# Performance work log

Hardware: AMD Instinct MI355X
Metric: run time of the kernel (lower is better)

Reference implementation:

```python
import jax, jax.numpy as jnp
import numpy as np

EPS = 1e-5  # torch BatchNorm2d default eps


def _conv(x, w, pad=0, groups=1):
    # x: NCHW, w: OIHW (torch layout); matches nn.Conv2d with given padding/groups
    return jax.lax.conv_general_dilated(
        x, w, window_strides=(1, 1), padding=[(pad, pad), (pad, pad)],
        dimension_numbers=("NCHW", "OIHW", "NCHW"), feature_group_count=groups)


def _bn_train(x, gamma, beta):
    # BatchNorm2d in training mode: batch stats over (N,H,W), biased variance
    m = jnp.mean(x, axis=(0, 2, 3), keepdims=True)
    v = jnp.mean(jnp.square(x - m), axis=(0, 2, 3), keepdims=True)
    return (x - m) * jax.lax.rsqrt(v + EPS) * gamma.reshape(1, -1, 1, 1) + beta.reshape(1, -1, 1, 1)


def setup_inputs() -> dict:
    key = jax.random.key(0)
    ks = jax.random.split(key, 8)
    B, C, H, W = 8, 32, 128, 128
    D = 8                      # num_directions
    WC = C * D                 # wavelet_channels = 256
    MID = WC * 2               # 512
    x = jax.random.normal(ks[0], (B, C, H, W), jnp.float32)
    # grouped directional filter bank: Conv2d(C, C*D, k=5, groups=C, bias=False)
    w_dir = jax.random.normal(ks[1], (WC, 1, 5, 5), jnp.float32) / np.sqrt(25.0)
    # wavelet_conv: Conv(WC->MID,3) BN ReLU Conv(MID->WC,3) BN ReLU
    w1 = jax.random.normal(ks[2], (MID, WC, 3, 3), jnp.float32) / np.sqrt(WC * 9.0)
    b1 = jnp.zeros((MID,), jnp.float32)
    g1 = jnp.ones((MID,), jnp.float32)
    be1 = jnp.zeros((MID,), jnp.float32)
    w2 = jax.random.normal(ks[3], (WC, MID, 3, 3), jnp.float32) / np.sqrt(MID * 9.0)
    b2 = jnp.zeros((WC,), jnp.float32)
    g2 = jnp.ones((WC,), jnp.float32)
    be2 = jnp.zeros((WC,), jnp.float32)
    # inverse_conv: Conv2d(WC, C, 1)
    w_inv = jax.random.normal(ks[4], (C, WC, 1, 1), jnp.float32) / np.sqrt(float(WC))
    b_inv = jnp.zeros((C,), jnp.float32)
    return {"x": x, "w_dir": w_dir, "w1": w1, "b1": b1, "g1": g1, "be1": be1,
            "w2": w2, "b2": b2, "g2": g2, "be2": be2, "w_inv": w_inv, "b_inv": b_inv}


def reference(x, w_dir, w1, b1, g1, be1, w2, b2, g2, be2, w_inv, b_inv):
    C = x.shape[1]
    # directional wavelet: grouped conv C -> C*8, k=5, pad=2, no bias
    coeffs = _conv(x, w_dir, pad=2, groups=C)                      # (B, 8C, H, W)
    # wavelet-domain conv stack
    h = _conv(coeffs, w1, pad=1) + b1.reshape(1, -1, 1, 1)         # (B, 16C, H, W)
    h = jax.nn.relu(_bn_train(h, g1, be1))
    h = _conv(h, w2, pad=1) + b2.reshape(1, -1, 1, 1)              # (B, 8C, H, W)
    h = jax.nn.relu(_bn_train(h, g2, be2))
    # inverse 1x1 conv back to C channels
    return _conv(h, w_inv) + b_inv.reshape(1, -1, 1, 1)            # (B, C, H, W)
```

## Files before the change

kernel.cpp:

```cpp
#include <hip/hip_runtime.h>

typedef unsigned short u16;
typedef unsigned int   u32;
typedef __attribute__((ext_vector_type(8)))  __bf16 bf16x8;
typedef __attribute__((ext_vector_type(4)))  float  f32x4;
typedef __attribute__((ext_vector_type(16))) float  f32x16;

__device__ __forceinline__ float bf2f(u16 u) {
    union { u32 i; float f; } v; v.i = ((u32)u) << 16; return v.f;
}
__device__ __forceinline__ u16 f2bf(float f) {
    u32 u = __float_as_uint(f);
    u32 r = (u + 0x7FFFu + ((u >> 16) & 1u)) >> 16;
    return (u16)r;
}

__device__ __forceinline__ void gl16(const u16* g, u16* l) {
    __builtin_amdgcn_global_load_lds(
        (const __attribute__((address_space(1))) unsigned int*)g,
        (__attribute__((address_space(3))) unsigned int*)l, 16, 0, 0);
}

__global__ __launch_bounds__(256) void dir_conv_k(const float* __restrict__ x,
                                                  const float* __restrict__ wd,
                                                  u16* __restrict__ coeffs) {
    int bid = blockIdx.x;
    int cc = bid & 3, y = (bid >> 2) & 127, n = bid >> 9;
    __shared__ float lx[5280];
    __shared__ float lw[1600];
    int t = threadIdx.x;
    for (int i = t; i < 1600; i += 256) {
        int ol = i / 25, tap = i - ol * 25;
        lw[tap * 64 + ol] = wd[(cc * 64 + ol) * 25 + tap];
    }
    for (int i = t; i < 5280; i += 256) {
        int c = i / 660, rem = i - c * 660;
        int ky = rem / 132, xx = rem - ky * 132;
        int gy = y - 2 + ky, gx = xx - 2;
        float v = 0.f;
        if (gy >= 0 && gy < 128 && gx >= 0 && gx < 128)
            v = x[(((n * 32 + cc * 8 + c) * 128 + gy) << 7) + gx];
        lx[i] = v;
    }
    __syncthreads();
    int px = t >> 1, oh = t & 1;
    float acc[4][8];
#pragma unroll
    for (int j = 0; j < 4; ++j)
#pragma unroll
        for (int d = 0; d < 8; ++d) acc[j][d] = 0.f;
#pragma unroll
    for (int j = 0; j < 4; ++j) {
        int cl = oh * 4 + j;
        const float* lxc = &lx[cl * 660];
#pragma unroll
        for (int ky = 0; ky < 5; ++ky)
#pragma unroll
            for (int kx = 0; kx < 5; ++kx) {
                float xv = lxc[ky * 132 + px + kx];
                const float* w8 = &lw[(ky * 5 + kx) * 64 + cl * 8];
#pragma unroll
                for (int d = 0; d < 8; ++d) acc[j][d] += xv * w8[d];
            }
    }
    long base = ((long)((n * 128 + y) * 128 + px)) * 256 + cc * 64 + oh * 32;
#pragma unroll
    for (int j = 0; j < 4; ++j) {
        uint4 o;
        o.x = (u32)f2bf(acc[j][0]) | ((u32)f2bf(acc[j][1]) << 16);
        o.y = (u32)f2bf(acc[j][2]) | ((u32)f2bf(acc[j][3]) << 16);
        o.z = (u32)f2bf(acc[j][4]) | ((u32)f2bf(acc[j][5]) << 16);
        o.w = (u32)f2bf(acc[j][6]) | ((u32)f2bf(acc[j][7]) << 16);
        *(uint4*)(coeffs + base + j * 8) = o;
    }
}

__global__ __launch_bounds__(256) void repack_w_k(const float* __restrict__ w,
                                                  u16* __restrict__ wp,
                                                  int OC, int IC, int total) {
    int f = blockIdx.x * 256 + threadIdx.x;
    if (f >= total) return;
    int KC = IC >> 5;
    int j  = f & 7;
    int h  = (f >> 3) & 1;
    int g  = f >> 4;
    int oc = g % OC; g /= OC;
    int s  = g & 1;  g >>= 1;
    int kc = g % KC;
    int tap = g / KC;
    int ic = kc * 32 + s * 16 + h * 8 + j;
    wp[f] = f2bf(w[(oc * IC + ic) * 9 + tap]);
}

template<int IC, int OC>
__global__ __launch_bounds__(256, 2) void conv3_k(const u16* __restrict__ base,
                                                  u32 in_off,
                                                  const u16* __restrict__ wp,
                                                  const float* __restrict__ bias,
                                                  u32 zp_off,
                                                  u16* __restrict__ outp,
                                                  float* __restrict__ statp) {
    constexpr int KC = IC / 32;
    constexpr int W  = 130;
    constexpr int TU = 12 * W;
    constexpr int NFULL = TU / 256;
    constexpr int REM   = TU % 256;
    __shared__ u16 lA0[TU * 8];
    __shared__ u16 lA1[TU * 8];

    int bx0 = blockIdx.x;
    int bx = ((bx0 & 7) << 7) + (bx0 >> 3);
    int y = bx & 127, n = bx >> 7;
    int ocb = blockIdx.y;
    int t = threadIdx.x, lane = t & 63, wv = t >> 6;
    int lm = lane & 31, h = lane >> 5;
    int ocw = ocb * 256 + wv * 64;

    u32 off[NFULL + 1];
#pragma unroll
    for (int i = 0; i <= NFULL; ++i) {
        int u = (i == NFULL) ? (NFULL * 256 + lane) : (i * 256 + t);
        int icq = u / (3 * W);
        int r2  = u - icq * (3 * W);
        int dy  = r2 / W;
        int xx  = r2 - dy * W;
        int gy = y - 1 + dy, gx = xx - 1;
        bool ok = ((unsigned)gy < 128u) && ((unsigned)gx < 128u);
        off[i] = ok ? (in_off + (u32)((n * 128 + gy) * 128 + gx) * IC + (icq & 3) * 8)
                    : zp_off;
    }

    auto stage = [&](u16* dst, int kc) {
#pragma unroll
        for (int i = 0; i < NFULL; ++i)
            gl16(base + off[i] + kc * 32, dst + (i * 256 + wv * 64) * 8);
        if (wv == 0 && lane < REM)
            gl16(base + off[NFULL] + kc * 32, dst + NFULL * 256 * 8);
    };

    u32 wboff = (u32)(ocw + lm) * 16 + h * 8;
    bf16x8 Ar[2][4];
    bf16x8 Br[2][2];

    {
        const u16* wb = wp + wboff;
        Br[0][0] = *(const bf16x8*)wb;
        Br[0][1] = *(const bf16x8*)(wb + 512);
    }

    f32x16 acc[4][2];
#pragma unroll
    for (int mf = 0; mf < 4; ++mf)
#pragma unroll
        for (int nf = 0; nf < 2; ++nf)
#pragma unroll
            for (int r = 0; r < 16; ++r) acc[mf][nf][r] = 0.f;

    stage(lA0, 0);
    for (int kc = 0; kc < KC; ++kc) {
        const u16* lAu = (kc & 1) ? lA1 : lA0;
        u16*       lAn = (kc & 1) ? lA0 : lA1;
        __syncthreads();
        {
            int au = ((h * 3) * W + lm) * 8;
            Ar[0][0] = *(const bf16x8*)(lAu + au);
            Ar[0][1] = *(const bf16x8*)(lAu + au + 256);
            Ar[0][2] = *(const bf16x8*)(lAu + au + 512);
            Ar[0][3] = *(const bf16x8*)(lAu + au + 768);
        }
        if (kc + 1 < KC) stage(lAn, kc + 1);
#pragma unroll
        for (int i = 0; i < 18; ++i) {
            const int j   = (i + 1) % 18;
            const int jdy = j / 6, jdx = (j % 6) >> 1, js = j & 1;
            const int jkc = (i == 17) ? ((kc + 1 < KC) ? kc + 1 : 0) : kc;
            if (i != 17) {
                int au = (((js * 2 + h) * 3 + jdy) * W + jdx + lm) * 8;
                Ar[j & 1][0] = *(const bf16x8*)(lAu + au);
                Ar[j & 1][1] = *(const bf16x8*)(lAu + au + 256);
                Ar[j & 1][2] = *(const bf16x8*)(lAu + au + 512);
                Ar[j & 1][3] = *(const bf16x8*)(lAu + au + 768);
            }
            {
                const u16* wb = wp + wboff
                    + (u32)(((jdy * 3 + jdx) * KC + jkc) * 2 + js) * (OC * 16);
                Br[j & 1][0] = *(const bf16x8*)wb;
                Br[j & 1][1] = *(const bf16x8*)(wb + 512);
            }
            __builtin_amdgcn_s_setprio(1);
            acc[0][0] = __builtin_amdgcn_mfma_f32_32x32x16_bf16(Ar[i & 1][0], Br[i & 1][0], acc[0][0], 0, 0, 0);
            acc[0][1] = __builtin_amdgcn_mfma_f32_32x32x16_bf16(Ar[i & 1][0], Br[i & 1][1], acc[0][1], 0, 0, 0);
            acc[1][0] = __builtin_amdgcn_mfma_f32_32x32x16_bf16(Ar[i & 1][1], Br[i & 1][0], acc[1][0], 0, 0, 0);
            acc[1][1] = __builtin_amdgcn_mfma_f32_32x32x16_bf16(Ar[i & 1][1], Br[i & 1][1], acc[1][1], 0, 0, 0);
            acc[2][0] = __builtin_amdgcn_mfma_f32_32x32x16_bf16(Ar[i & 1][2], Br[i & 1][0], acc[2][0], 0, 0, 0);
            acc[2][1] = __builtin_amdgcn_mfma_f32_32x32x16_bf16(Ar[i & 1][2], Br[i & 1][1], acc[2][1], 0, 0, 0);
            acc[3][0] = __builtin_amdgcn_mfma_f32_32x32x16_bf16(Ar[i & 1][3], Br[i & 1][0], acc[3][0], 0, 0, 0);
            acc[3][1] = __builtin_amdgcn_mfma_f32_32x32x16_bf16(Ar[i & 1][3], Br[i & 1][1], acc[3][1], 0, 0, 0);
            __builtin_amdgcn_s_setprio(0);
        }
    }

    long rowb = (long)(n * 128 + y) * 128;
    float ss[2] = {0.f, 0.f}, qq[2] = {0.f, 0.f};
#pragma unroll
    for (int nf = 0; nf < 2; ++nf) {
        int oc = ocw + nf * 32 + lm;
        float bi = bias[oc];
#pragma unroll
        for (int mf = 0; mf < 4; ++mf)
#pragma unroll
            for (int r = 0; r < 16; ++r) {
                int px = mf * 32 + (r & 3) + ((r >> 2) << 3) + (h << 2);
                u16 bv = f2bf(acc[mf][nf][r] + bi);
                outp[(rowb + px) * OC + oc] = bv;
                float vr = bf2f(bv);
                ss[nf] += vr;
                qq[nf] += vr * vr;
            }
    }
#pragma unroll
    for (int nf = 0; nf < 2; ++nf) {
        ss[nf] += __shfl_xor(ss[nf], 32);
        qq[nf] += __shfl_xor(qq[nf], 32);
    }
    if (h == 0) {
#pragma unroll
        for (int nf = 0; nf < 2; ++nf) {
            int oc = ocw + nf * 32 + lm;
            atomicAdd(&statp[oc * 2],     ss[nf]);
            atomicAdd(&statp[oc * 2 + 1], qq[nf]);
        }
    }
}

template<int C>
__global__ __launch_bounds__(256) void stats2_k(const float* __restrict__ part,
                                                const float* __restrict__ g,
                                                const float* __restrict__ be,
                                                float* __restrict__ ab) {
    int ch = blockIdx.x * 256 + threadIdx.x;
    if (ch >= C) return;
    float s = part[ch * 2], q = part[ch * 2 + 1];
    const float M = 131072.f;
    float mean = s / M;
    float var = q / M - mean * mean;
    float a = g[ch] * rsqrtf(var + 1e-5f);
    ab[ch * 2]     = a;
    ab[ch * 2 + 1] = be[ch] - mean * a;
}

__global__ __launch_bounds__(256) void bn_relu_k(u16* __restrict__ h,
                                                 const float* __restrict__ ab) {
    long idx8 = (long)blockIdx.x * 256 + threadIdx.x;
    u16* p = h + idx8 * 8;
    uint4 v = *(const uint4*)p;
    int chb = ((int)idx8 & 63) << 3;
    u32 w[4] = {v.x, v.y, v.z, v.w};
    u32 o[4];
#pragma unroll
    for (int q = 0; q < 4; ++q) {
        int ch = chb + q * 2;
        float2 a0 = *(const float2*)(ab + ch * 2);
        float2 a1 = *(const float2*)(ab + ch * 2 + 2);
        float f0 = bf2f((u16)(w[q] & 0xffff));
        float f1 = bf2f((u16)(w[q] >> 16));
        f0 = fmaxf(f0 * a0.x + a0.y, 0.f);
        f1 = fmaxf(f1 * a1.x + a1.y, 0.f);
        o[q] = (u32)f2bf(f0) | ((u32)f2bf(f1) << 16);
    }
    *(uint4*)p = make_uint4(o[0], o[1], o[2], o[3]);
}

__global__ __launch_bounds__(256) void inv_conv_k(const u16* __restrict__ h2,
                                                  const float* __restrict__ ab,
                                                  const float* __restrict__ winv,
                                                  const float* __restrict__ binv,
                                                  float* __restrict__ out) {
    __shared__ float lw[8192];
    __shared__ float lab[512];
    int t = threadIdx.x;
    for (int i = t; i < 8192; i += 256) {
        int k = i >> 5, oc = i & 31;
        lw[i] = winv[oc * 256 + k];
    }
    lab[t] = ab[t];
    lab[t + 256] = ab[t + 256];
    __syncthreads();
    long p = (long)blockIdx.x * 256 + t;
    const u16* hp = h2 + p * 256;
    f32x4 acc[8];
    f32x4 zero = {0.f, 0.f, 0.f, 0.f};
#pragma unroll
    for (int q = 0; q < 8; ++q) acc[q] = zero;
    for (int k = 0; k < 256; k += 8) {
        uint4 hv = *(const uint4*)(hp + k);
        u32 wv[4] = {hv.x, hv.y, hv.z, hv.w};
#pragma unroll
        for (int e = 0; e < 8; ++e) {
            u16 us = (e & 1) ? (u16)(wv[e >> 1] >> 16) : (u16)(wv[e >> 1] & 0xffff);
            int kk = k + e;
            float v = bf2f(us);
            v = fmaxf(v * lab[kk * 2] + lab[kk * 2 + 1], 0.f);
            const f32x4* w4 = (const f32x4*)(lw + kk * 32);
#pragma unroll
            for (int q = 0; q < 8; ++q) acc[q] += v * w4[q];
        }
    }
    int n = (int)(p >> 14), rem = (int)(p & 16383);
#pragma unroll
    for (int q = 0; q < 8; ++q)
#pragma unroll
        for (int c = 0; c < 4; ++c) {
            int oc = q * 4 + c;
            out[((long)(n * 32 + oc) << 14) + rem] = acc[q][c] + binv[oc];
        }
}

extern "C" void kernel_launch(void* const* d_in, const int* in_sizes, int n_in,
                              void* d_out, int out_size, void* d_ws, size_t ws_size,
                              hipStream_t stream) {
    const float* x     = (const float*)d_in[0];
    const float* w_dir = (const float*)d_in[1];
    const float* w1    = (const float*)d_in[2];
    const float* b1    = (const float*)d_in[3];
    const float* g1    = (const float*)d_in[4];
    const float* be1   = (const float*)d_in[5];
    const float* w2    = (const float*)d_in[6];
    const float* b2    = (const float*)d_in[7];
    const float* g2    = (const float*)d_in[8];
    const float* be2   = (const float*)d_in[9];
    const float* w_inv = (const float*)d_in[10];
    const float* b_inv = (const float*)d_in[11];
    float* out = (float*)d_out;
    char* ws = (char*)d_ws;

    u16*   w1p   = (u16*)(ws + 0);
    u16*   w2p   = (u16*)(ws + 2359296);
    float* part1 = (float*)(ws + 4718592);
    float* part2 = (float*)(ws + 4722688);
    float* ab1   = (float*)(ws + 5242880);
    float* ab2   = (float*)(ws + 5246976);
    u16*   zp    = (u16*)(ws + 5249024);
    u16*   coef  = (u16*)(ws + 8388608);
    u16*   h1    = (u16*)(ws + 75497472);
    const u16* basep = (const u16*)ws;
    u32 zp_off   = 5249024 / 2;
    u32 coef_off = 8388608 / 2;
    u32 h1_off   = 75497472 / 2;

    hipMemsetAsync(zp, 0, 1024, stream);
    hipMemsetAsync(part1, 0, 8192, stream);
    repack_w_k<<<4608, 256, 0, stream>>>(w1, w1p, 512, 256, 1179648);
    repack_w_k<<<4608, 256, 0, stream>>>(w2, w2p, 256, 512, 1179648);
    dir_conv_k<<<4096, 256, 0, stream>>>(x, w_dir, coef);
    conv3_k<256, 512><<<dim3(1024, 2), 256, 0, stream>>>(basep, coef_off, w1p, b1, zp_off, h1, part1);
    stats2_k<512><<<2, 256, 0, stream>>>(part1, g1, be1, ab1);
    bn_relu_k<<<32768, 256, 0, stream>>>(h1, ab1);
    conv3_k<512, 256><<<dim3(1024, 1), 256, 0, stream>>>(basep, h1_off, w2p, b2, zp_off, coef, part2);
    stats2_k<256><<<1, 256, 0, stream>>>(part2, g2, be2, ab2);
    inv_conv_k<<<512, 256, 0, stream>>>(coef, ab2, w_inv, b_inv, out);
}
```

Before: 729.7 us.

## Process two output rows per 512-thread block with barrier-phased conv pipeline

The 3x3 implicit-GEMM conv kernel now uses 512 threads per block covering two output rows. Waves split into 2 row-groups by 4 OC-groups, so a 4-row input halo tile is shared instead of each row reloading 3 rows. Each K-chunk is restructured into 9 phases: paired LDS A-reads, double-buffered weight loads, interleaved global-to-LDS staging, explicit s_waitcnt and barriers, then 16 MFMAs. This cuts input halo traffic and tries to overlap loads with MFMA, at the cost of many more block-wide barriers and higher register pressure at 512 threads with 2 blocks per CU.

New measurement: 798.8 us. +9.5%, slower.

```diff
diff --git a/kernel.cpp b/kernel.cpp
--- a/kernel.cpp
+++ b/kernel.cpp
@@ -92,8 +92,82 @@
     wp[f] = f2bf(w[(oc * IC + ic) * 9 + tap]);
 }
 
+#define MFMA8(A4, B2)                                                          \
+    {                                                                          \
+        acc[0][0] = __builtin_amdgcn_mfma_f32_32x32x16_bf16(A4[0], B2[0], acc[0][0], 0, 0, 0); \
+        acc[0][1] = __builtin_amdgcn_mfma_f32_32x32x16_bf16(A4[0], B2[1], acc[0][1], 0, 0, 0); \
+        acc[1][0] = __builtin_amdgcn_mfma_f32_32x32x16_bf16(A4[1], B2[0], acc[1][0], 0, 0, 0); \
+        acc[1][1] = __builtin_amdgcn_mfma_f32_32x32x16_bf16(A4[1], B2[1], acc[1][1], 0, 0, 0); \
+        acc[2][0] = __builtin_amdgcn_mfma_f32_32x32x16_bf16(A4[2], B2[0], acc[2][0], 0, 0, 0); \
+        acc[2][1] = __builtin_amdgcn_mfma_f32_32x32x16_bf16(A4[2], B2[1], acc[2][1], 0, 0, 0); \
+        acc[3][0] = __builtin_amdgcn_mfma_f32_32x32x16_bf16(A4[3], B2[0], acc[3][0], 0, 0, 0); \
+        acc[3][1] = __builtin_amdgcn_mfma_f32_32x32x16_bf16(A4[3], B2[1], acc[3][1], 0, 0, 0); \
+    }
+
+#define AREAD(dst, lAu, S, DY, DX)                                             \
+    {                                                                          \
+        int au_ = ((((S) * 2 + h) * 4 + (wm + (DY))) * 130 + (DX) + lm) * 8;   \
+        dst[0] = *(const bf16x8*)((lAu) + au_);                                \
+        dst[1] = *(const bf16x8*)((lAu) + au_ + 256);                          \
+        dst[2] = *(const bf16x8*)((lAu) + au_ + 512);                          \
+        dst[3] = *(const bf16x8*)((lAu) + au_ + 768);                          \
+    }
+
+#define BLOAD(dst, DY, DX, S, KCV)                                             \
+    {                                                                          \
+        const u16* wpk_ = wp + ((u32)((((DY) * 3 + (DX)) * KC + (KCV)) * 2 + (S)) * (u32)(OC * 16)); \
+        dst[0] = *(const bf16x8*)(wpk_ + wboff);                               \
+        dst[1] = *(const bf16x8*)(wpk_ + wboff + 512);                         \
+    }
+
+#define KCBODY(KCV, OFF)                                                       \
+    {                                                                          \
+        const int kc_ = (KCV);                                                 \
+        const u16* lAu = (kc_ & 1) ? lA1 : lA0;                                \
+        u16*       lAn = (kc_ & 1) ? lA0 : lA1;                                \
+        const bool doStage = (kc_ + 1 < KC);                                   \
+        asm volatile("s_waitcnt vmcnt(4)" ::: "memory");                       \
+        __builtin_amdgcn_s_barrier();                                          \
+        _Pragma("unroll")                                                      \
+        for (int p = 0; p < 9; ++p) {                                          \
+            const int sa = 2 * p, sb = 2 * p + 1;                              \
+            AREAD(Ar[0], lAu, (sa & 1), (sa / 6), ((sa % 6) >> 1));            \
+            AREAD(Ar[1], lAu, (sb & 1), (sb / 6), ((sb % 6) >> 1));            \
+            const int na = (2 * p + 2) % 18, nb = (2 * p + 3) % 18;            \
+            int kcN = (p == 8) ? (doStage ? kc_ + 1 : 0) : kc_;                \
+            if (((p + (OFF)) & 1) == 0) {                                      \
+                BLOAD(BrB[0], (na / 6), ((na % 6) >> 1), (na & 1), kcN);       \
+                BLOAD(BrB[1], (nb / 6), ((nb % 6) >> 1), (nb & 1), kcN);       \
+            } else {                                                           \
+                BLOAD(BrA[0], (na / 6), ((na % 6) >> 1), (na & 1), kcN);       \
+                BLOAD(BrA[1], (nb / 6), ((nb % 6) >> 1), (nb & 1), kcN);       \
+            }                                                                  \
+            if (p < NFULL) {                                                   \
+                if (doStage)                                                   \
+                    gl16(base + off[p] + (kc_ + 1) * 32, lAn + (p * 512 + wv * 64) * 8); \
+            }                                                                  \
+            if (p == NFULL) {                                                  \
+                if (doStage && wv == 0 && lane < REM)                          \
+                    gl16(base + off[NFULL] + (kc_ + 1) * 32, lAn + NFULL * 512 * 8); \
+            }                                                                  \
+            __builtin_amdgcn_s_barrier();                                      \
+            asm volatile("s_waitcnt lgkmcnt(0)" ::: "memory");                 \
+            __builtin_amdgcn_sched_barrier(0);                                 \
+            __builtin_amdgcn_s_setprio(1);                                     \
+            if (((p + (OFF)) & 1) == 0) {                                      \
+                MFMA8(Ar[0], BrA[0]);                                          \
+                MFMA8(Ar[1], BrA[1]);                                          \
+            } else {                                                           \
+                MFMA8(Ar[0], BrB[0]);                                          \
+                MFMA8(Ar[1], BrB[1]);                                          \
+            }                                                                  \
+            __builtin_amdgcn_s_setprio(0);                                     \
+            __builtin_amdgcn_s_barrier();                                      \
+        }                                                                      \
+    }
+
 template<int IC, int OC>
-__global__ __launch_bounds__(256, 2) void conv3_k(const u16* __restrict__ base,
+__global__ __launch_bounds__(512, 2) void conv3_k(const u16* __restrict__ base,
                                                   u32 in_off,
                                                   const u16* __restrict__ wp,
                                                   const float* __restrict__ bias,
@@ -101,106 +175,62 @@
                                                   u16* __restrict__ outp,
                                                   float* __restrict__ statp) {
     constexpr int KC = IC / 32;
-    constexpr int W  = 130;
-    constexpr int TU = 12 * W;
-    constexpr int NFULL = TU / 256;
-    constexpr int REM   = TU % 256;
+    constexpr int TU = 4 * 4 * 130;
+    constexpr int NFULL = TU / 512;
+    constexpr int REM   = TU % 512;
     __shared__ u16 lA0[TU * 8];
     __shared__ u16 lA1[TU * 8];
 
     int bx0 = blockIdx.x;
-    int bx = ((bx0 & 7) << 7) + (bx0 >> 3);
-    int y = bx & 127, n = bx >> 7;
+    int bx = ((bx0 & 7) << 6) + (bx0 >> 3);
+    int yp = bx & 63, n = bx >> 6;
+    int y0 = yp * 2;
     int ocb = blockIdx.y;
     int t = threadIdx.x, lane = t & 63, wv = t >> 6;
+    int wm = wv & 1, wn = wv >> 1;
     int lm = lane & 31, h = lane >> 5;
-    int ocw = ocb * 256 + wv * 64;
+    int ocw = ocb * 256 + wn * 64;
+    u32 wboff = (u32)(ocw + lm) * 16 + h * 8;
 
     u32 off[NFULL + 1];
 #pragma unroll
     for (int i = 0; i <= NFULL; ++i) {
-        int u = (i == NFULL) ? (NFULL * 256 + lane) : (i * 256 + t);
-        int icq = u / (3 * W);
-        int r2  = u - icq * (3 * W);
-        int dy  = r2 / W;
-        int xx  = r2 - dy * W;
-        int gy = y - 1 + dy, gx = xx - 1;
+        int u = (i == NFULL) ? (NFULL * 512 + lane) : (i * 512 + t);
+        int icq = u / 520;
+        int r2  = u - icq * 520;
+        int row = r2 / 130;
+        int xx  = r2 - row * 130;
+        int gy = y0 - 1 + row, gx = xx - 1;
         bool ok = ((unsigned)gy < 128u) && ((unsigned)gx < 128u);
         off[i] = ok ? (in_off + (u32)((n * 128 + gy) * 128 + gx) * IC + (icq & 3) * 8)
                     : zp_off;
     }
 
-    auto stage = [&](u16* dst, int kc) {
-#pragma unroll
-        for (int i = 0; i < NFULL; ++i)
-            gl16(base + off[i] + kc * 32, dst + (i * 256 + wv * 64) * 8);
-        if (wv == 0 && lane < REM)
-            gl16(base + off[NFULL] + kc * 32, dst + NFULL * 256 * 8);
-    };
-
-    u32 wboff = (u32)(ocw + lm) * 16 + h * 8;
+    f32x16 acc[4][2];
+#pragma unroll
+    for (int mf = 0; mf < 4; ++mf)
+#pragma unroll
+        for (int nf = 0; nf < 2; ++nf)
+#pragma unroll
+            for (int r = 0; r < 16; ++r) acc[mf][nf][r] = 0.f;
+
     bf16x8 Ar[2][4];
-    bf16x8 Br[2][2];
-
-    {
-        const u16* wb = wp + wboff;
-        Br[0][0] = *(const bf16x8*)wb;
-        Br[0][1] = *(const bf16x8*)(wb + 512);
-    }
-
-    f32x16 acc[4][2];
-#pragma unroll
-    for (int mf = 0; mf < 4; ++mf)
-#pragma unroll
-        for (int nf = 0; nf < 2; ++nf)
-#pragma unroll
-            for (int r = 0; r < 16; ++r) acc[mf][nf][r] = 0.f;
-
-    stage(lA0, 0);
-    for (int kc = 0; kc < KC; ++kc) {
-        const u16* lAu = (kc & 1) ? lA1 : lA0;
-        u16*       lAn = (kc & 1) ? lA0 : lA1;
-        __syncthreads();
-        {
-            int au = ((h * 3) * W + lm) * 8;
-            Ar[0][0] = *(const bf16x8*)(lAu + au);
-            Ar[0][1] = *(const bf16x8*)(lAu + au + 256);
-            Ar[0][2] = *(const bf16x8*)(lAu + au + 512);
-            Ar[0][3] = *(const bf16x8*)(lAu + au + 768);
-        }
-        if (kc + 1 < KC) stage(lAn, kc + 1);
-#pragma unroll
-        for (int i = 0; i < 18; ++i) {
-            const int j   = (i + 1) % 18;
-            const int jdy = j / 6, jdx = (j % 6) >> 1, js = j & 1;
-            const int jkc = (i == 17) ? ((kc + 1 < KC) ? kc + 1 : 0) : kc;
-            if (i != 17) {
-                int au = (((js * 2 + h) * 3 + jdy) * W + jdx + lm) * 8;
-                Ar[j & 1][0] = *(const bf16x8*)(lAu + au);
-                Ar[j & 1][1] = *(const bf16x8*)(lAu + au + 256);
-                Ar[j & 1][2] = *(const bf16x8*)(lAu + au + 512);
-                Ar[j & 1][3] = *(const bf16x8*)(lAu + au + 768);
-            }
-            {
-                const u16* wb = wp + wboff
-                    + (u32)(((jdy * 3 + jdx) * KC + jkc) * 2 + js) * (OC * 16);
-                Br[j & 1][0] = *(const bf16x8*)wb;
-                Br[j & 1][1] = *(const bf16x8*)(wb + 512);
-            }
-            __builtin_amdgcn_s_setprio(1);
-            acc[0][0] = __builtin_amdgcn_mfma_f32_32x32x16_bf16(Ar[i & 1][0], Br[i & 1][0], acc[0][0], 0, 0, 0);
-            acc[0][1] = __builtin_amdgcn_mfma_f32_32x32x16_bf16(Ar[i & 1][0], Br[i & 1][1], acc[0][1], 0, 0, 0);
-            acc[1][0] = __builtin_amdgcn_mfma_f32_32x32x16_bf16(Ar[i & 1][1], Br[i & 1][0], acc[1][0], 0, 0, 0);
-            acc[1][1] = __builtin_amdgcn_mfma_f32_32x32x16_bf16(Ar[i & 1][1], Br[i & 1][1], acc[1][1], 0, 0, 0);
-            acc[2][0] = __builtin_amdgcn_mfma_f32_32x32x16_bf16(Ar[i & 1][2], Br[i & 1][0], acc[2][0], 0, 0, 0);
-            acc[2][1] = __builtin_amdgcn_mfma_f32_32x32x16_bf16(Ar[i & 1][2], Br[i & 1][1], acc[2][1], 0, 0, 0);
-            acc[3][0] = __builtin_amdgcn_mfma_f32_32x32x16_bf16(Ar[i & 1][3], Br[i & 1][0], acc[3][0], 0, 0, 0);
-            acc[3][1] = __builtin_amdgcn_mfma_f32_32x32x16_bf16(Ar[i & 1][3], Br[i & 1][1], acc[3][1], 0, 0, 0);
-            __builtin_amdgcn_s_setprio(0);
-        }
-    }
-
-    long rowb = (long)(n * 128 + y) * 128;
+    bf16x8 BrA[2][2], BrB[2][2];
+
+#pragma unroll
+    for (int i = 0; i < NFULL; ++i)
+        gl16(base + off[i], lA0 + (i * 512 + wv * 64) * 8);
+    if (wv == 0 && lane < REM)
+        gl16(base + off[NFULL], lA0 + NFULL * 512 * 8);
+    BLOAD(BrA[0], 0, 0, 0, 0);
+    BLOAD(BrA[1], 0, 0, 1, 0);
+
+    for (int kcb = 0; kcb < KC; kcb += 2) {
+        KCBODY(kcb, 0);
+        KCBODY(kcb + 1, 1);
+    }
+
+    long rowb = (long)(n * 128 + y0 + wm) * 128;
     float ss[2] = {0.f, 0.f}, qq[2] = {0.f, 0.f};
 #pragma unroll
     for (int nf = 0; nf < 2; ++nf) {
@@ -353,10 +383,10 @@
     repack_w_k<<<4608, 256, 0, stream>>>(w1, w1p, 512, 256, 1179648);
     repack_w_k<<<4608, 256, 0, stream>>>(w2, w2p, 256, 512, 1179648);
     dir_conv_k<<<4096, 256, 0, stream>>>(x, w_dir, coef);
-    conv3_k<256, 512><<<dim3(1024, 2), 256, 0, stream>>>(basep, coef_off, w1p, b1, zp_off, h1, part1);
+    conv3_k<256, 512><<<dim3(512, 2), 512, 0, stream>>>(basep, coef_off, w1p, b1, zp_off, h1, part1);
     stats2_k<512><<<2, 256, 0, stream>>>(part1, g1, be1, ab1);
     bn_relu_k<<<32768, 256, 0, stream>>>(h1, ab1);
-    conv3_k<512, 256><<<dim3(1024, 1), 256, 0, stream>>>(basep, h1_off, w2p, b2, zp_off, coef, part2);
+    conv3_k<512, 256><<<dim3(512, 1), 512, 0, stream>>>(basep, h1_off, w2p, b2, zp_off, coef, part2);
     stats2_k<256><<<1, 256, 0, stream>>>(part2, g2, be2, ab2);
     inv_conv_k<<<512, 256, 0, stream>>>(coef, ab2, w_inv, b_inv, out);
 }
```
